# Performance work log

Hardware: AMD Instinct MI355X
Metric: run time of the kernel (lower is better)

The kernel has to match this reference:

```python
import jax, jax.numpy as jnp
import numpy as np

# ---- config (matches init_kwargs) ----
GROUP_NUM = 2048
K_NEIGHBORS = 32
OUT_DIM = 192
SIGMA, BASELINE, SCALING, EPS = 0.26, 0.1, 10.0, 1e-6
ALPHA, BETA = 1000.0, 100.0
ADAPTIVE_RATIO = 0.5
IN_DIM = 3
ADAPTIVE_DIM = int(OUT_DIM * ADAPTIVE_RATIO)          # 96
FOURIER_DIM = OUT_DIM - ADAPTIVE_DIM                  # 96
FEAT_DIM_F = FOURIER_DIM // (IN_DIM * 2)              # 16
FEAT_DIM_A = int(np.ceil(ADAPTIVE_DIM / IN_DIM))      # 32
FEAT_NUM_A = FEAT_DIM_A * IN_DIM                      # 96
OUT_IDX = np.linspace(0, FEAT_NUM_A - 1, ADAPTIVE_DIM).astype(np.int64)


def setup_inputs() -> dict:
    key = jax.random.key(0)
    k1, k2, k3, k4 = jax.random.split(key, 4)
    xyz = jax.random.normal(k1, (4, 8192, 3), dtype=jnp.float32)
    x = jax.random.normal(k2, (4, 8192, 96), dtype=jnp.float32)
    bn_gamma = jax.random.uniform(k3, (192,), dtype=jnp.float32)
    bn_beta = jax.random.normal(k4, (192,), dtype=jnp.float32)
    return {"xyz": xyz, "x": x, "bn_gamma": bn_gamma, "bn_beta": bn_beta}


def _fps(xyz, m):
    """Farthest point sampling. xyz: [B,N,3] -> idx [B,m] (int32). Seed = index 0."""
    def single(pts):
        n = pts.shape[0]
        def step(carry, _):
            dists, last = carry
            d = jnp.sum((pts - pts[last]) ** 2, axis=-1)
            dists = jnp.minimum(dists, d)
            nxt = jnp.argmax(dists).astype(jnp.int32)
            return (dists, nxt), nxt
        init = (jnp.full((n,), 1e10, pts.dtype), jnp.array(0, jnp.int32))
        _, idxs = jax.lax.scan(step, init, None, length=m - 1)
        return jnp.concatenate([jnp.zeros((1,), jnp.int32), idxs])
    return jax.vmap(single)(xyz)


def _square_distance(src, dst):
    # src: [B,S,3], dst: [B,N,3] -> [B,S,N]
    d = -2.0 * jnp.einsum('bsc,bnc->bsn', src, dst)
    d += jnp.sum(src ** 2, -1)[:, :, None]
    d += jnp.sum(dst ** 2, -1)[:, None, :]
    return d


def _gather_knn(points, idx):
    # points: [B,N,C], idx: [B,G,K] -> [B,G,K,C]
    return jax.vmap(lambda p, i: p[i])(points, idx)


def _forward(xyz, x, bn_gamma, bn_beta):
    B, N, _ = xyz.shape
    G, K = GROUP_NUM, K_NEIGHBORS

    # ---- Grouper_seg ----
    fps_idx = _fps(xyz, G)                                   # [B,G]
    lc_xyz = jnp.take_along_axis(xyz, fps_idx[..., None], 1)  # [B,G,3]
    lc_x = jnp.take_along_axis(x, fps_idx[..., None], 1)      # [B,G,C]
    sqr = _square_distance(lc_xyz, xyz)                       # [B,G,N]
    knn_idx = jax.lax.top_k(-sqr, K)[1]                       # [B,G,K] smallest-k
    knn_xyz = _gather_knn(xyz, knn_idx)                       # [B,G,K,3]
    knn_x = _gather_knn(x, knn_idx)                           # [B,G,K,C]

    # ---- Aggregation_seg: local normalization ----
    mean_x = lc_x[:, :, None, :]
    std_x = jnp.std(knn_x - mean_x, ddof=1)
    mean_xyz = lc_xyz[:, :, None, :]
    std_xyz = jnp.std(knn_xyz - mean_xyz, ddof=1)
    knn_x = (knn_x - mean_x) / (std_x + 1e-5)
    knn_xyz_n = (knn_xyz - mean_xyz) / (std_xyz + 1e-5)       # [B,G,K,3]
    C = knn_x.shape[-1]
    knn_x = jnp.concatenate(
        [knn_x, jnp.broadcast_to(lc_x[:, :, None, :], (B, G, K, C))], axis=-1)  # [B,G,K,2C]
    knn_xyz_cf = jnp.transpose(knn_xyz_n, (0, 3, 1, 2))       # [B,3,G,K]
    knn_x_cf = jnp.transpose(knn_x, (0, 3, 1, 2))             # [B,OUT_DIM,G,K]

    # ---- PosE_Geo: fourier part ----
    feat_range = jnp.arange(FEAT_DIM_F, dtype=knn_xyz_cf.dtype)
    dim_embed = ALPHA ** (feat_range / FEAT_DIM_F)            # [F]
    div = BETA * knn_xyz_cf[..., None] / dim_embed            # [B,3,G,K,F]
    fourier = jnp.stack([jnp.sin(div), jnp.cos(div)], axis=-1)  # [B,3,G,K,F,2]
    fourier = fourier.reshape(B, IN_DIM, G, K, 2 * FEAT_DIM_F)
    fourier = jnp.transpose(fourier, (0, 1, 4, 2, 3)).reshape(B, FOURIER_DIM, G, K)

    # ---- AdaptiveEmbedding (parameterless, data-driven) ----
    x4 = knn_xyz_n                                            # [B,G,K,3]
    gstd = jnp.mean(jnp.std(x4.reshape(B, -1, IN_DIM), axis=1, ddof=1))
    sig = SIGMA * (1.0 + gstd) + EPS
    blend = jax.nn.sigmoid((gstd - BASELINE) * SCALING)
    feat_val = jnp.linspace(-1.0, 1.0, FEAT_DIM_A + 2)[1:-1]  # [Fa]
    z = (x4[..., None] - feat_val) / sig                      # [B,G,K,3,Fa]
    comb = blend * jnp.exp(-0.5 * z * z) + (1.0 - blend) * jnp.cos(z)
    ae = comb.reshape(B, G, K, FEAT_NUM_A)[..., OUT_IDX]      # [B,G,K,ADAPTIVE_DIM]
    ae_cf = jnp.transpose(ae, (0, 3, 1, 2))                   # [B,ADAPTIVE_DIM,G,K]

    pe = jnp.concatenate([fourier, ae_cf], axis=1)            # [B,OUT_DIM,G,K]
    knn_x_w = (knn_x_cf + pe) * pe

    # ---- Pooling_seg: max+mean pool, BatchNorm1d (train stats) + GELU ----
    lc = jnp.max(knn_x_w, -1) + jnp.mean(knn_x_w, -1)         # [B,OUT_DIM,G]
    mu = jnp.mean(lc, axis=(0, 2), keepdims=True)
    var = jnp.var(lc, axis=(0, 2), keepdims=True)
    y = (lc - mu) / jnp.sqrt(var + 1e-5)
    y = y * bn_gamma[None, :, None] + bn_beta[None, :, None]
    return jax.nn.gelu(y, approximate=False)


def reference(xyz, x, bn_gamma, bn_beta):
    return _forward(xyz, x, bn_gamma, bn_beta)
```

## Files before the change

kernel.cpp:

```cpp
#include <hip/hip_runtime.h>
#include <cstdint>
#include <math.h>

#define NPTS 8192
#define NB 4
#define NG 2048
#define NK 32
#define CIN 96
#define COUT 192

typedef unsigned long long ull;

__global__ __launch_bounds__(256) void setup_kernel(const float* __restrict__ xyz,
                                                    float* __restrict__ xs, float* __restrict__ ys,
                                                    float* __restrict__ zs, float* __restrict__ d2){
  int i = blockIdx.x*256 + threadIdx.x;
  if (i >= NB*NPTS) return;
  float x = xyz[3*i+0], y = xyz[3*i+1], z = xyz[3*i+2];
  xs[i]=x; ys[i]=y; zs[i]=z;
  d2[i] = __fadd_rn(__fadd_rn(__fmul_rn(x,x),__fmul_rn(y,y)),__fmul_rn(z,z));
}

template<int CTRL>
__device__ __forceinline__ void dppmax_pair(unsigned& hi, unsigned& lo){
  unsigned ohi = (unsigned)__builtin_amdgcn_update_dpp((int)hi, (int)hi, CTRL, 0xf, 0xf, false);
  unsigned olo = (unsigned)__builtin_amdgcn_update_dpp((int)lo, (int)lo, CTRL, 0xf, 0xf, false);
  bool gt = (ohi > hi) || (ohi == hi && olo > lo);
  hi = gt ? ohi : hi;
  lo = gt ? olo : lo;
}

__device__ __forceinline__ ull umax64(ull a, ull b){ return (a > b) ? a : b; }

__device__ __forceinline__ float bbox_lb(float lx, float ly, float lz,
                                         float x0, float x1, float y0, float y1,
                                         float z0, float z1){
#pragma clang fp contract(off)
  float qx = fminf(fmaxf(lx,x0),x1);
  float qy = fminf(fmaxf(ly,y0),y1);
  float qz = fminf(fmaxf(lz,z0),z1);
  float dx = qx-lx, dy = qy-ly, dz = qz-lz;
  return (dx*dx+dy*dy)+dz*dz;
}

__global__ __launch_bounds__(512,2) void fps_kernel(const float* __restrict__ xyz, int* __restrict__ fps_idx){
#pragma clang fp contract(off)
  extern __shared__ char smem[];
  float4* ctab = (float4*)smem;
  ull*    keys = (ull*)(smem + 131072);
  int*    hist = (int*)(smem + 131072 + 128);
  float*  bbs  = (float*)(smem + 131072 + 128 + 2048);
  const int b = blockIdx.x, t = threadIdx.x;
  const int w = t>>6, lane = t&63;
  const float* base = xyz + (size_t)b*NPTS*3;

  float ox[16], oy[16], oz[16];
#pragma unroll
  for (int j=0;j<16;++j){
    int p = t + 512*j;
    ox[j]=base[3*p+0]; oy[j]=base[3*p+1]; oz[j]=base[3*p+2];
  }
  float mnx=ox[0],mxx=ox[0],mny=oy[0],mxy=oy[0],mnz=oz[0],mxz=oz[0];
#pragma unroll
  for (int j=1;j<16;++j){
    mnx=fminf(mnx,ox[j]); mxx=fmaxf(mxx,ox[j]);
    mny=fminf(mny,oy[j]); mxy=fmaxf(mxy,oy[j]);
    mnz=fminf(mnz,oz[j]); mxz=fmaxf(mxz,oz[j]);
  }
#pragma unroll
  for (int off=32; off>0; off>>=1){
    mnx=fminf(mnx,__shfl_xor(mnx,off)); mxx=fmaxf(mxx,__shfl_xor(mxx,off));
    mny=fminf(mny,__shfl_xor(mny,off)); mxy=fmaxf(mxy,__shfl_xor(mxy,off));
    mnz=fminf(mnz,__shfl_xor(mnz,off)); mxz=fmaxf(mxz,__shfl_xor(mxz,off));
  }
  hist[t] = 0;
  if (lane==0){
    bbs[w*6+0]=mnx; bbs[w*6+1]=mxx; bbs[w*6+2]=mny;
    bbs[w*6+3]=mxy; bbs[w*6+4]=mnz; bbs[w*6+5]=mxz;
  }
  if (t==0) fps_idx[b*NG] = 0;
  __syncthreads();
  float gx0=1e30f,gx1=-1e30f,gy0=1e30f,gy1=-1e30f,gz0=1e30f,gz1=-1e30f;
  for (int q=0;q<8;++q){
    gx0=fminf(gx0,bbs[q*6+0]); gx1=fmaxf(gx1,bbs[q*6+1]);
    gy0=fminf(gy0,bbs[q*6+2]); gy1=fmaxf(gy1,bbs[q*6+3]);
    gz0=fminf(gz0,bbs[q*6+4]); gz1=fmaxf(gz1,bbs[q*6+5]);
  }
  const float sxv = 8.0f/fmaxf(gx1-gx0,1e-20f);
  const float syv = 8.0f/fmaxf(gy1-gy0,1e-20f);
  const float szv = 8.0f/fmaxf(gz1-gz0,1e-20f);
  int cell[16];
#pragma unroll
  for (int j=0;j<16;++j){
    int cx = min(7,(int)((ox[j]-gx0)*sxv));
    int cy = min(7,(int)((oy[j]-gy0)*syv));
    int cz = min(7,(int)((oz[j]-gz0)*szv));
    int m = (cx&1) | ((cy&1)<<1) | ((cz&1)<<2)
          | ((cx&2)<<2) | ((cy&2)<<3) | ((cz&2)<<4)
          | ((cx&4)<<4) | ((cy&4)<<5) | ((cz&4)<<6);
    cell[j]=m;
    atomicAdd(&hist[m],1);
  }
  __syncthreads();
  if (t < 64){
    int s0[8];
#pragma unroll
    for (int j=0;j<8;++j) s0[j]=hist[t*8+j];
    int tot=0;
#pragma unroll
    for (int j=0;j<8;++j){ int v=s0[j]; s0[j]=tot; tot+=v; }
    int inc=tot;
#pragma unroll
    for (int off=1; off<64; off<<=1){
      int o=__shfl_up(inc,off);
      if (t>=off) inc+=o;
    }
    int excl=inc-tot;
#pragma unroll
    for (int j=0;j<8;++j) hist[t*8+j]=excl+s0[j];
  }
  __syncthreads();
#pragma unroll
  for (int j=0;j<16;++j){
    int pos = atomicAdd(&hist[cell[j]],1);
    ctab[pos] = make_float4(ox[j],oy[j],oz[j], __int_as_float(t+512*j));
  }
  __syncthreads();
  float D[16]; unsigned lowb[16];
  float hx0[2],hx1[2],hy0[2],hy1[2],hz0[2],hz1[2];
#pragma unroll
  for (int j=0;j<16;++j){
    int pos = (w<<10) + (j<<6) + lane;
    float4 c4 = ctab[pos];
    unsigned orig = (unsigned)__float_as_int(c4.w);
    lowb[j] = ((8191u-orig)<<13) | (unsigned)pos;
    D[j] = 1e10f;
    const int h = j>>3;
    if ((j&7)==0){ hx0[h]=c4.x; hx1[h]=c4.x; hy0[h]=c4.y; hy1[h]=c4.y; hz0[h]=c4.z; hz1[h]=c4.z; }
    else {
      hx0[h]=fminf(hx0[h],c4.x); hx1[h]=fmaxf(hx1[h],c4.x);
      hy0[h]=fminf(hy0[h],c4.y); hy1[h]=fmaxf(hy1[h],c4.y);
      hz0[h]=fminf(hz0[h],c4.z); hz1[h]=fmaxf(hz1[h],c4.z);
    }
  }
#pragma unroll
  for (int h=0;h<2;++h){
#pragma unroll
    for (int off=32; off>0; off>>=1){
      hx0[h]=fminf(hx0[h],__shfl_xor(hx0[h],off)); hx1[h]=fmaxf(hx1[h],__shfl_xor(hx1[h],off));
      hy0[h]=fminf(hy0[h],__shfl_xor(hy0[h],off)); hy1[h]=fmaxf(hy1[h],__shfl_xor(hy1[h],off));
      hz0[h]=fminf(hz0[h],__shfl_xor(hz0[h],off)); hz1[h]=fmaxf(hz1[h],__shfl_xor(hz1[h],off));
    }
  }
  const float bx0=fminf(hx0[0],hx0[1]), bx1=fmaxf(hx1[0],hx1[1]);
  const float by0=fminf(hy0[0],hy0[1]), by1=fmaxf(hy1[0],hy1[1]);
  const float bz0=fminf(hz0[0],hz0[1]), bz1=fmaxf(hz1[0],hz1[1]);

  float lx=base[0], ly=base[1], lz=base[2];
  float Mw = 1e10f;
  unsigned mylow = 0;
  for (int it=0; it<NG-1; ++it){
    const float thr = Mw*1.0001f;
    float LB = bbox_lb(lx,ly,lz, bx0,bx1,by0,by1,bz0,bz1);
    ull* kslot = &keys[(it&1)*8 + w];
    if (LB <= thr){
      float LB0 = bbox_lb(lx,ly,lz, hx0[0],hx1[0],hy0[0],hy1[0],hz0[0],hz1[0]);
      float LB1 = bbox_lb(lx,ly,lz, hx0[1],hx1[1],hy0[1],hy1[1],hz0[1],hz1[1]);
      if (LB0 <= thr){
#pragma unroll
        for (int j=0;j<8;++j){
          float4 c4 = ctab[(w<<10) + (j<<6) + lane];
          float dx=c4.x-lx, dy=c4.y-ly, dz=c4.z-lz;
          float d=(dx*dx+dy*dy)+dz*dz;
          D[j]=fminf(D[j],d);
        }
      }
      if (LB1 <= thr){
#pragma unroll
        for (int j=8;j<16;++j){
          float4 c4 = ctab[(w<<10) + (j<<6) + lane];
          float dx=c4.x-lx, dy=c4.y-ly, dz=c4.z-lz;
          float d=(dx*dx+dy*dy)+dz*dz;
          D[j]=fminf(D[j],d);
        }
      }
      float bd=-1.0f;
#pragma unroll
      for (int j=0;j<16;++j) bd=fmaxf(bd,D[j]);
      unsigned bl=0;
#pragma unroll
      for (int j=0;j<16;++j){
        unsigned c2 = (lowb[j]>bl)?lowb[j]:bl;
        bl = (D[j]==bd) ? c2 : bl;
      }
      unsigned hi = __float_as_uint(bd), lo = bl;
      dppmax_pair<0x111>(hi,lo); dppmax_pair<0x112>(hi,lo); dppmax_pair<0x114>(hi,lo);
      dppmax_pair<0x118>(hi,lo); dppmax_pair<0x142>(hi,lo); dppmax_pair<0x143>(hi,lo);
      unsigned hw  = (unsigned)__builtin_amdgcn_readlane((int)hi,63);
      unsigned lwv = (unsigned)__builtin_amdgcn_readlane((int)lo,63);
      if (lane==63) *kslot = (((ull)hw)<<32) | (ull)lwv;
      Mw = __uint_as_float(hw);
      mylow = lwv;
    } else {
      if (lane==63) *kslot = (((ull)__float_as_uint(Mw))<<32) | (ull)mylow;
    }
    __syncthreads();
    const ulonglong2* kk2 = (const ulonglong2*)(keys + (it&1)*8);
    ulonglong2 p0 = kk2[0], p1 = kk2[1], p2 = kk2[2], p3 = kk2[3];
    ull a0 = umax64(p0.x, p0.y), a1 = umax64(p1.x, p1.y);
    ull a2 = umax64(p2.x, p2.y), a3 = umax64(p3.x, p3.y);
    ull k  = umax64(umax64(a0,a1), umax64(a2,a3));
    unsigned lw = (unsigned)k;
    float4 c4 = ctab[lw & 0x1FFFu];
    lx=c4.x; ly=c4.y; lz=c4.z;
    if (t==0) fps_idx[b*NG + it + 1] = (int)(8191u - ((lw>>13)&0x1FFFu));
  }
}

__device__ __forceinline__ bool lexlt(float ad, int ai, float bd, int bi){
  return (ad < bd) || ((ad == bd) && (ai < bi));
}
__device__ __forceinline__ void sort_desc(float& d, int& i, int lane){
#pragma unroll
  for (int k=2;k<=64;k<<=1){
#pragma unroll
    for (int j=k>>1;j>0;j>>=1){
      float od = __shfl_xor(d, j);
      int   oi = __shfl_xor(i, j);
      bool dirUp = (lane & k) != 0;
      bool lower = (lane & j) == 0;
      bool less  = lexlt(d,i,od,oi);
      bool keep  = (less == (lower == dirUp));
      if (!keep){ d=od; i=oi; }
    }
  }
}
__device__ __forceinline__ void merge_asc(float& d, int& i, int lane){
#pragma unroll
  for (int j=32;j>0;j>>=1){
    float od = __shfl_xor(d, j);
    int   oi = __shfl_xor(i, j);
    bool lower = (lane & j) == 0;
    bool less  = lexlt(d,i,od,oi);
    bool keep  = (less == lower);
    if (!keep){ d=od; i=oi; }
  }
}

__global__ __launch_bounds__(256) void knn_kernel(const float* __restrict__ xs, const float* __restrict__ ys,
                                                  const float* __restrict__ zs, const float* __restrict__ d2,
                                                  const int* __restrict__ fps_idx, int* __restrict__ knn_out){
  __shared__ float tx[256], ty[256], tz[256], td[256];
  const int tid = threadIdx.x;
  const int wid = tid>>6, lane = tid&63;
  const int pid = blockIdx.x*4 + wid;
  const int b = pid >> 11;
  const float* bx = xs + b*NPTS;
  const float* by = ys + b*NPTS;
  const float* bz = zs + b*NPTS;
  const float* bD = d2 + b*NPTS;
  const int fi = fps_idx[pid];
  const float ax = bx[fi], ay = by[fi], az = bz[fi];
  const float src2 = __fadd_rn(__fadd_rn(__fmul_rn(ax,ax),__fmul_rn(ay,ay)),__fmul_rn(az,az));
  float Ad = INFINITY; int Ai = 0x7fffffff;
  float tau_d = INFINITY; int tau_i = 0x7fffffff;
  for (int s=0; s<NPTS/256; ++s){
    __syncthreads();
    int gidx = s*256 + tid;
    tx[tid]=bx[gidx]; ty[tid]=by[gidx]; tz[tid]=bz[gidx]; td[tid]=bD[gidx];
    __syncthreads();
    float m0,m1,m2,m3; int i0,i1,i2,i3;
#define LOADJ(mj, ij, J) { int li = (J)*64 + lane; \
    float dot = __fadd_rn(__fadd_rn(__fmul_rn(ax,tx[li]),__fmul_rn(ay,ty[li])),__fmul_rn(az,tz[li])); \
    mj = __fadd_rn(__fadd_rn(__fmul_rn(-2.0f,dot), src2), td[li]); ij = s*256 + li; }
    LOADJ(m0,i0,0) LOADJ(m1,i1,1) LOADJ(m2,i2,2) LOADJ(m3,i3,3)
#undef LOADJ
    while (true){
      bool any = lexlt(m0,i0,tau_d,tau_i) || lexlt(m1,i1,tau_d,tau_i) ||
                 lexlt(m2,i2,tau_d,tau_i) || lexlt(m3,i3,tau_d,tau_i);
      if (__ballot(any) == 0ull) break;
      float cd = m0; int ci = i0; int sel = 0;
      if (lexlt(m1,i1,cd,ci)){ cd=m1; ci=i1; sel=1; }
      if (lexlt(m2,i2,cd,ci)){ cd=m2; ci=i2; sel=2; }
      if (lexlt(m3,i3,cd,ci)){ cd=m3; ci=i3; sel=3; }
      if      (sel==0) m0=INFINITY;
      else if (sel==1) m1=INFINITY;
      else if (sel==2) m2=INFINITY;
      else             m3=INFINITY;
      sort_desc(cd, ci, lane);
      if (lexlt(cd,ci,Ad,Ai)){ Ad=cd; Ai=ci; }
      merge_asc(Ad, Ai, lane);
      tau_d = __shfl(Ad, 31);
      tau_i = __shfl(Ai, 31);
    }
  }
  if (lane < NK) knn_out[pid*NK + lane] = Ai;
}

__global__ __launch_bounds__(256) void stats_kernel(const float* __restrict__ x, const float* __restrict__ xyz,
                                                    const int* __restrict__ fps_idx, const int* __restrict__ knn,
                                                    double* __restrict__ partials){
  const int tid=threadIdx.x, wid=tid>>6, lane=tid&63;
  const int pid = blockIdx.x*4 + wid;
  const int b = pid>>11;
  const int fi = fps_idx[pid];
  const float* xb = x + (size_t)b*NPTS*CIN;
  const float* zb = xyz + (size_t)b*NPTS*3;
  const float lc0 = xb[fi*CIN + lane];
  float lc1 = 0.f; if (lane<32) lc1 = xb[fi*CIN + 64 + lane];
  float czv = 0.f; if (lane<3)  czv = zb[fi*3 + lane];
  double s1=0.0, s2=0.0, a1=0.0, a2=0.0;
  for (int k=0;k<NK;++k){
    int idx = knn[pid*NK + k];
    float d0 = __fsub_rn(xb[idx*CIN + lane], lc0);
    s1 += (double)d0; s2 += (double)d0*(double)d0;
    if (lane<32){
      float d1 = __fsub_rn(xb[idx*CIN + 64 + lane], lc1);
      s1 += (double)d1; s2 += (double)d1*(double)d1;
    }
    if (lane<3){
      float w = __fsub_rn(zb[idx*3 + lane], czv);
      a1 += (double)w; a2 += (double)w*(double)w;
    }
  }
#pragma unroll
  for (int off=32; off>0; off>>=1){ s1 += __shfl_xor(s1,off); s2 += __shfl_xor(s2,off); }
  __shared__ double shx[4][2];
  __shared__ double shz[4][3][2];
  if (lane==0){ shx[wid][0]=s1; shx[wid][1]=s2; }
  if (lane<3){ shz[wid][lane][0]=a1; shz[wid][lane][1]=a2; }
  __syncthreads();
  if (tid==0){
    double u0=0,u1=0;
    for (int w=0;w<4;++w){ u0+=shx[w][0]; u1+=shx[w][1]; }
    double* outp = partials + (size_t)blockIdx.x*8;
    outp[0]=u0; outp[1]=u1;
    for (int axq=0; axq<3; ++axq){
      double v0=0,v1=0;
      for (int w=0;w<4;++w){ v0+=shz[w][axq][0]; v1+=shz[w][axq][1]; }
      outp[2+2*axq]=v0; outp[3+2*axq]=v1;
    }
  }
}

__global__ void finalize_kernel(const double* __restrict__ partials, float* __restrict__ scal){
  const int lane = threadIdx.x;
  double s1=0,s2=0;
  double z0a=0,z0b=0,z1a=0,z1b=0,z2a=0,z2b=0;
  for (int i=0;i<32;++i){
    const double* p = partials + (size_t)(lane*32+i)*8;
    s1+=p[0]; s2+=p[1];
    z0a+=p[2]; z0b+=p[3]; z1a+=p[4]; z1b+=p[5]; z2a+=p[6]; z2b+=p[7];
  }
#pragma unroll
  for (int off=32; off>0; off>>=1){ s1+=__shfl_xor(s1,off); s2+=__shfl_xor(s2,off); }
#pragma unroll
  for (int off=8; off>0; off>>=1){
    z0a+=__shfl_xor(z0a,off); z0b+=__shfl_xor(z0b,off);
    z1a+=__shfl_xor(z1a,off); z1b+=__shfl_xor(z1b,off);
    z2a+=__shfl_xor(z2a,off); z2b+=__shfl_xor(z2b,off);
  }
  __shared__ double zb[4][3][2];
  if ((lane&15)==0){
    int b = lane>>4;
    zb[b][0][0]=z0a; zb[b][0][1]=z0b;
    zb[b][1][0]=z1a; zb[b][1][1]=z1b;
    zb[b][2][0]=z2a; zb[b][2][1]=z2b;
  }
  __syncthreads();
  if (lane==0){
    double nx = (double)NB*NG*NK*CIN;
    double varx = (s2 - s1*s1/nx)/(nx-1.0);
    float stdx = (float)sqrt(varx);
    double t1=0,t2=0;
    for (int b=0;b<4;++b) for (int a=0;a<3;++a){ t1+=zb[b][a][0]; t2+=zb[b][a][1]; }
    double nz = (double)NB*NG*NK*3;
    double varz = (t2 - t1*t1/nz)/(nz-1.0);
    float stdz = (float)sqrt(varz);
    float sdiv = stdz + 1e-5f;
    double n2 = (double)NG*NK;
    double acc=0.0;
    for (int b=0;b<4;++b) for (int a=0;a<3;++a){
      double v = (zb[b][a][1] - zb[b][a][0]*zb[b][a][0]/n2)/(n2-1.0);
      acc += sqrt(v);
    }
    float gstd = (float)(acc/12.0) / sdiv;
    float sig = 0.26f*(1.0f+gstd) + 1e-6f;
    float blend = 1.0f/(1.0f + expf(-(gstd-0.1f)*10.0f));
    scal[0] = 1.0f/(stdx + 1e-5f);
    scal[1] = 1.0f/sdiv;
    scal[2] = 1.0f/sig;
    scal[3] = blend;
  }
}

__global__ __launch_bounds__(256) void main_kernel(const float* __restrict__ x, const float* __restrict__ xyz,
                                                   const int* __restrict__ fps_idx, const int* __restrict__ knn,
                                                   const float* __restrict__ scal, float* __restrict__ lc_out){
  const int tid=threadIdx.x, wid=tid>>6, lane=tid&63;
  const int pid = blockIdx.x*4 + wid;
  const int b = pid>>11, g = pid&2047;
  const float inv_x = scal[0], inv_z = scal[1], inv_sig = scal[2], blend = scal[3];
  const float omb = 1.0f - blend;
  const int fi = fps_idx[pid];
  const float* xb = x + (size_t)b*NPTS*CIN;
  const float* zb = xyz + (size_t)b*NPTS*3;
  const float cx = zb[fi*3+0], cy = zb[fi*3+1], cz = zb[fi*3+2];
  const float lcx0 = xb[fi*CIN + lane];
  const float lcx1 = (lane<32) ? xb[fi*CIN + 64 + lane] : xb[fi*CIN + lane - 32];
  const float lcx2 = xb[fi*CIN + 32 + lane];
  const int dim0 = lane>>5;
  const int rr0 = lane&31;
  const bool cos0 = rr0 & 1;
  const float bs0 = 100.0f / powf(1000.0f, (float)(rr0>>1) * (1.0f/16.0f));
  const bool cos1 = lane & 1;
  const float bs1 = 100.0f / powf(1000.0f, (float)((lane&31)>>1) * (1.0f/16.0f));
  const float fv1 = (float)(-1.0 + 2.0*(double)(lane-32+1)/33.0);
  const int dim2 = (32+lane)>>5;
  const int j2 = (32+lane)&31;
  const float fv2 = (float)(-1.0 + 2.0*(double)(j2+1)/33.0);

  float mx0=-INFINITY, mx1=-INFINITY, mx2=-INFINITY;
  float sm0=0.f, sm1=0.f, sm2=0.f;
  for (int k=0;k<NK;++k){
    const int idx = knn[pid*NK + k];
    const float p0 = zb[idx*3+0], p1 = zb[idx*3+1], p2v = zb[idx*3+2];
    const float xn0 = (p0-cx)*inv_z, xn1 = (p1-cy)*inv_z, xn2 = (p2v-cz)*inv_z;
    const float xk0 = xb[idx*CIN + lane];
    float xk1 = 0.f; if (lane<32) xk1 = xb[idx*CIN + 64 + lane];
    {
      float v = dim0 ? xn1 : xn0;
      float a = v * bs0;
      float pe = cos0 ? __cosf(a) : __sinf(a);
      float f = (xk0 - lcx0) * inv_x;
      float w = (f + pe) * pe;
      mx0 = fmaxf(mx0, w); sm0 += w;
    }
    {
      float pe, f;
      if (lane < 32){
        float a = xn2 * bs1;
        pe = cos1 ? __cosf(a) : __sinf(a);
        f = (xk1 - lcx1) * inv_x;
      } else {
        float zq = (xn0 - fv1) * inv_sig;
        pe = blend * __expf(-0.5f*zq*zq) + omb * __cosf(zq);
        f = lcx1;
      }
      float w = (f + pe) * pe;
      mx1 = fmaxf(mx1, w); sm1 += w;
    }
    {
      float v = (dim2==1) ? xn1 : xn2;
      float zq = (v - fv2) * inv_sig;
      float pe = blend * __expf(-0.5f*zq*zq) + omb * __cosf(zq);
      float w = (lcx2 + pe) * pe;
      mx2 = fmaxf(mx2, w); sm2 += w;
    }
  }
  const size_t obase = ((size_t)b*COUT)*NG + g;
  lc_out[obase + (size_t)lane*NG]       = mx0 + sm0*(1.0f/32.0f);
  lc_out[obase + (size_t)(64+lane)*NG]  = mx1 + sm1*(1.0f/32.0f);
  lc_out[obase + (size_t)(128+lane)*NG] = mx2 + sm2*(1.0f/32.0f);
}

__global__ __launch_bounds__(256) void bn_stats_kernel(const float* __restrict__ lc, float* __restrict__ bn){
  const int c = blockIdx.x, t = threadIdx.x, lane=t&63, wid=t>>6;
  double s1=0.0, s2=0.0;
  for (int i=t; i<NB*NG; i+=256){
    int b=i>>11, g=i&2047;
    float v = lc[((size_t)(b*COUT)+c)*NG + g];
    s1 += (double)v; s2 += (double)v*(double)v;
  }
#pragma unroll
  for (int off=32; off>0; off>>=1){ s1+=__shfl_xor(s1,off); s2+=__shfl_xor(s2,off); }
  __shared__ double sh1[4], sh2[4];
  if (lane==0){ sh1[wid]=s1; sh2[wid]=s2; }
  __syncthreads();
  if (t==0){
    double a=sh1[0]+sh1[1]+sh1[2]+sh1[3], q=sh2[0]+sh2[1]+sh2[2]+sh2[3];
    double n=(double)(NB*NG);
    double mu=a/n, var=q/n - mu*mu;
    bn[c]=(float)mu;
    bn[COUT+c]=(float)(1.0/sqrt(var + 1e-5));
  }
}

__global__ __launch_bounds__(256) void final_kernel(const float* __restrict__ bn, const float* __restrict__ gamma,
                                                    const float* __restrict__ beta, float* __restrict__ out){
  int i = blockIdx.x*256 + threadIdx.x;
  int c = (i >> 11) % COUT;
  float v = out[i];
  float y = (v - bn[c]) * bn[COUT + c];
  y = y*gamma[c] + beta[c];
  out[i] = y * 0.5f * (1.0f + erff(y * 0.70710678118654752f));
}

extern "C" void kernel_launch(void* const* d_in, const int* in_sizes, int n_in,
                              void* d_out, int out_size, void* d_ws, size_t ws_size,
                              hipStream_t stream){
  const float* xyz   = (const float*)d_in[0];
  const float* x     = (const float*)d_in[1];
  const float* gamma = (const float*)d_in[2];
  const float* beta  = (const float*)d_in[3];
  float* out = (float*)d_out;
  char* ws = (char*)d_ws;
  int*    fps  = (int*)   (ws + 0);
  int*    knn  = (int*)   (ws + 32768);
  float*  xs   = (float*) (ws + 1081344);
  float*  ys   = (float*) (ws + 1212416);
  float*  zs   = (float*) (ws + 1343488);
  float*  d2   = (float*) (ws + 1474560);
  double* parts= (double*)(ws + 1605632);
  float*  scal = (float*) (ws + 1736704);
  float*  bn   = (float*) (ws + 1736768);

  const int fps_lds = 131072 + 128 + 2048 + 192;
  (void)hipFuncSetAttribute(reinterpret_cast<const void*>(fps_kernel),
                            hipFuncAttributeMaxDynamicSharedMemorySize, fps_lds);

  setup_kernel   <<<dim3((NB*NPTS+255)/256), dim3(256), 0, stream>>>(xyz, xs, ys, zs, d2);
  fps_kernel     <<<dim3(NB),                dim3(512), fps_lds, stream>>>(xyz, fps);
  knn_kernel     <<<dim3(NB*NG/4),           dim3(256), 0, stream>>>(xs, ys, zs, d2, fps, knn);
  stats_kernel   <<<dim3(NB*NG/4),           dim3(256), 0, stream>>>(x, xyz, fps, knn, parts);
  finalize_kernel<<<dim3(1),                 dim3(64),  0, stream>>>(parts, scal);
  main_kernel    <<<dim3(NB*NG/4),           dim3(256), 0, stream>>>(x, xyz, fps, knn, scal, out);
  bn_stats_kernel<<<dim3(COUT),              dim3(256), 0, stream>>>(out, bn);
  final_kernel   <<<dim3((NB*COUT*NG)/256),  dim3(256), 0, stream>>>(bn, gamma, beta, out);
}
```

Baseline: 2.915 ms.

## Cache FPS point coords in registers and keep per-half running max

Each thread now holds its 16 candidate point coordinates in registers instead of re-reading them from LDS every FPS iteration. It also keeps a separate running max and argmax key for each half of its points, so a half whose bounding box is pruned reuses its cached max instead of being rescanned. When both halves are pruned, the wave skips the DPP reduction and just republishes its previous key. The cost is 48 more VGPRs per thread, which could lower occupancy or cause spills.

```diff
diff --git a/kernel.cpp b/kernel.cpp
--- a/kernel.cpp
+++ b/kernel.cpp
@@ -126,12 +126,13 @@
     ctab[pos] = make_float4(ox[j],oy[j],oz[j], __int_as_float(t+512*j));
   }
   __syncthreads();
-  float D[16]; unsigned lowb[16];
+  float px[16],py[16],pz[16],D[16]; unsigned lowb[16];
   float hx0[2],hx1[2],hy0[2],hy1[2],hz0[2],hz1[2];
 #pragma unroll
   for (int j=0;j<16;++j){
     int pos = (w<<10) + (j<<6) + lane;
     float4 c4 = ctab[pos];
+    px[j]=c4.x; py[j]=c4.y; pz[j]=c4.z;
     unsigned orig = (unsigned)__float_as_int(c4.w);
     lowb[j] = ((8191u-orig)<<13) | (unsigned)pos;
     D[j] = 1e10f;
@@ -156,6 +157,14 @@
   const float by0=fminf(hy0[0],hy0[1]), by1=fmaxf(hy1[0],hy1[1]);
   const float bz0=fminf(hz0[0],hz0[1]), bz1=fmaxf(hz1[0],hz1[1]);
 
+  float M0v = 1e10f, M1v = 1e10f;
+  unsigned L0v = 0, L1v = 0;
+#pragma unroll
+  for (int j=0;j<8;++j){
+    L0v = (lowb[j]   > L0v) ? lowb[j]   : L0v;
+    L1v = (lowb[j+8] > L1v) ? lowb[j+8] : L1v;
+  }
+
   float lx=base[0], ly=base[1], lz=base[2];
   float Mw = 1e10f;
   unsigned mylow = 0;
@@ -163,53 +172,71 @@
     const float thr = Mw*1.0001f;
     float LB = bbox_lb(lx,ly,lz, bx0,bx1,by0,by1,bz0,bz1);
     ull* kslot = &keys[(it&1)*8 + w];
+    bool wrote_new = false;
     if (LB <= thr){
       float LB0 = bbox_lb(lx,ly,lz, hx0[0],hx1[0],hy0[0],hy1[0],hz0[0],hz1[0]);
       float LB1 = bbox_lb(lx,ly,lz, hx0[1],hx1[1],hy0[1],hy1[1],hz0[1],hz1[1]);
-      if (LB0 <= thr){
-#pragma unroll
-        for (int j=0;j<8;++j){
-          float4 c4 = ctab[(w<<10) + (j<<6) + lane];
-          float dx=c4.x-lx, dy=c4.y-ly, dz=c4.z-lz;
-          float d=(dx*dx+dy*dy)+dz*dz;
-          D[j]=fminf(D[j],d);
+      const bool a0 = (LB0 <= thr), a1 = (LB1 <= thr);
+      if (a0 || a1){
+        if (a0){
+          float m = -1.0f;
+#pragma unroll
+          for (int j=0;j<8;++j){
+            float dx=px[j]-lx, dy=py[j]-ly, dz=pz[j]-lz;
+            float d=(dx*dx+dy*dy)+dz*dz;
+            float nd=fminf(D[j],d);
+            D[j]=nd;
+            m=fmaxf(m,nd);
+          }
+          unsigned L=0;
+#pragma unroll
+          for (int j=0;j<8;++j){
+            unsigned c2 = (lowb[j]>L)?lowb[j]:L;
+            L = (D[j]==m) ? c2 : L;
+          }
+          M0v=m; L0v=L;
         }
+        if (a1){
+          float m = -1.0f;
+#pragma unroll
+          for (int j=8;j<16;++j){
+            float dx=px[j]-lx, dy=py[j]-ly, dz=pz[j]-lz;
+            float d=(dx*dx+dy*dy)+dz*dz;
+            float nd=fminf(D[j],d);
+            D[j]=nd;
+            m=fmaxf(m,nd);
+          }
+          unsigned L=0;
+#pragma unroll
+          for (int j=8;j<16;++j){
+            unsigned c2 = (lowb[j]>L)?lowb[j]:L;
+            L = (D[j]==m) ? c2 : L;
+          }
+          M1v=m; L1v=L;
+        }
+        unsigned hi0=__float_as_uint(M0v), hi1=__float_as_uint(M1v);
+        bool g1 = (hi1>hi0) || (hi1==hi0 && L1v>L0v);
+        unsigned hi = g1?hi1:hi0;
+        unsigned lo = g1?L1v:L0v;
+        dppmax_pair<0x111>(hi,lo); dppmax_pair<0x112>(hi,lo); dppmax_pair<0x114>(hi,lo);
+        dppmax_pair<0x118>(hi,lo); dppmax_pair<0x142>(hi,lo); dppmax_pair<0x143>(hi,lo);
+        unsigned hw  = (unsigned)__builtin_amdgcn_readlane((int)hi,63);
+        unsigned lwv = (unsigned)__builtin_amdgcn_readlane((int)lo,63);
+        if (lane==63) *kslot = (((ull)hw)<<32) | (ull)lwv;
+        Mw = __uint_as_float(hw);
+        mylow = lwv;
+        wrote_new = true;
       }
-      if (LB1 <= thr){
-#pragma unroll
-        for (int j=8;j<16;++j){
-          float4 c4 = ctab[(w<<10) + (j<<6) + lane];
-          float dx=c4.x-lx, dy=c4.y-ly, dz=c4.z-lz;
-          float d=(dx*dx+dy*dy)+dz*dz;
-          D[j]=fminf(D[j],d);
-        }
-      }
-      float bd=-1.0f;
-#pragma unroll
-      for (int j=0;j<16;++j) bd=fmaxf(bd,D[j]);
-      unsigned bl=0;
-#pragma unroll
-      for (int j=0;j<16;++j){
-        unsigned c2 = (lowb[j]>bl)?lowb[j]:bl;
-        bl = (D[j]==bd) ? c2 : bl;
-      }
-      unsigned hi = __float_as_uint(bd), lo = bl;
-      dppmax_pair<0x111>(hi,lo); dppmax_pair<0x112>(hi,lo); dppmax_pair<0x114>(hi,lo);
-      dppmax_pair<0x118>(hi,lo); dppmax_pair<0x142>(hi,lo); dppmax_pair<0x143>(hi,lo);
-      unsigned hw  = (unsigned)__builtin_amdgcn_readlane((int)hi,63);
-      unsigned lwv = (unsigned)__builtin_amdgcn_readlane((int)lo,63);
-      if (lane==63) *kslot = (((ull)hw)<<32) | (ull)lwv;
-      Mw = __uint_as_float(hw);
-      mylow = lwv;
-    } else {
+    }
+    if (!wrote_new){
       if (lane==63) *kslot = (((ull)__float_as_uint(Mw))<<32) | (ull)mylow;
     }
     __syncthreads();
     const ulonglong2* kk2 = (const ulonglong2*)(keys + (it&1)*8);
     ulonglong2 p0 = kk2[0], p1 = kk2[1], p2 = kk2[2], p3 = kk2[3];
-    ull a0 = umax64(p0.x, p0.y), a1 = umax64(p1.x, p1.y);
-    ull a2 = umax64(p2.x, p2.y), a3 = umax64(p3.x, p3.y);
-    ull k  = umax64(umax64(a0,a1), umax64(a2,a3));
+    ull a0k = umax64(p0.x, p0.y), a1k = umax64(p1.x, p1.y);
+    ull a2k = umax64(p2.x, p2.y), a3k = umax64(p3.x, p3.y);
+    ull k  = umax64(umax64(a0k,a1k), umax64(a2k,a3k));
     unsigned lw = (unsigned)k;
     float4 c4 = ctab[lw & 0x1FFFu];
     lx=c4.x; ly=c4.y; lz=c4.z;
```

Result: faster. 2.611 ms (-10.4%).
